# Performance work log

Measured on AMD Instinct MI355X. Metric: run time of the kernel, lower is better.

The kernel has to match this reference:

```python
import jax, jax.numpy as jnp
import numpy as np

IN_DIM = 512
OUT_DIM = 512


def setup_inputs() -> dict:
    key = jax.random.key(0)
    ks = jax.random.split(key, 7)
    B, S = 4, 2048
    scale = 1.0 / np.sqrt(IN_DIM)
    X = jax.random.normal(ks[0], (B, S, IN_DIM), dtype=jnp.float32)
    Wq = jax.random.normal(ks[1], (IN_DIM, OUT_DIM), dtype=jnp.float32) * scale
    Wk = jax.random.normal(ks[2], (IN_DIM, OUT_DIM), dtype=jnp.float32) * scale
    Wv = jax.random.normal(ks[3], (IN_DIM, OUT_DIM), dtype=jnp.float32) * scale
    bq = jnp.zeros((OUT_DIM,), dtype=jnp.float32)
    bk = jnp.zeros((OUT_DIM,), dtype=jnp.float32)
    bv = jnp.zeros((OUT_DIM,), dtype=jnp.float32)
    return {"X": X, "Wq": Wq, "bq": bq, "Wk": Wk, "bk": bk, "Wv": Wv, "bv": bv}


def reference(X, Wq, bq, Wk, bk, Wv, bv):
    # Q/K/V projections: [B,S,in] @ [in,out] -> [B,S,out]
    Q = X @ Wq + bq
    K = X @ Wk + bk
    V = X @ Wv + bv
    d_k = jnp.asarray(Q.shape[-1], Q.dtype)
    # scores: [B,S,S] = QK^T / sqrt(d_k)
    scores = jnp.einsum('bsd,btd->bst', Q, K) / jnp.sqrt(d_k)
    attn = jax.nn.softmax(scores, axis=-1)
    # out: [B,S,out]
    return jnp.einsum('bst,btd->bsd', attn, V)
```

## Files before the change

### kernel.cpp

```cpp
#include <hip/hip_runtime.h>
#include <hip/hip_bf16.h>
#include <stdint.h>

#define SEQ   2048
#define DIM   512
#define BATCH 4

typedef __attribute__((ext_vector_type(8))) short  short8;
typedef __attribute__((ext_vector_type(4))) float  floatx4;

static __device__ __forceinline__ unsigned short f2b(float f) {
  return __builtin_bit_cast(unsigned short, __float2bfloat16(f));
}

static __device__ __forceinline__ void gll16(const void* g, void* l) {
  __builtin_amdgcn_global_load_lds(
      (__attribute__((address_space(1))) void*)(uintptr_t)g,
      (__attribute__((address_space(3))) void*)l, 16, 0, 0);
}


template <int AF, int BF, int WM, int WN, int KC, int KIT>
__device__ __forceinline__ void fgemm_pipe(
    const char* __restrict__ A, int rtA0, int TKA,
    const char* __restrict__ B, int rtB0, int TKB,
    char* lds, floatx4 (&acc)[AF / WM][BF / WN])
{
  constexpr int AWF  = AF / WM, BWF = BF / WN;
  constexpr int SLOT = (AF + BF) * KC * 1024;
  constexpr int L    = KC * (AF / 8 + BF / 8);
  static_assert(KIT >= 3, "pipeline needs >=3 K-steps");
  const int tid = threadIdx.x;
  const int w = tid >> 6, l = tid & 63;
  const int wm = w % WM, wn = w / WM;

  auto stage = [&](int slot, int kt) {
    char* dst = lds + slot * SLOT;
#pragma unroll
    for (int c = 0; c < KC; ++c) {
#pragma unroll
      for (int q = 0; q < AF / 8; ++q) {
        const int f = q * 8 + w;
        gll16(A + (((size_t)(rtA0 + f) * TKA + kt * KC + c) << 10) + l * 16,
              dst + (c * AF + f) * 1024 + l * 16);
      }
#pragma unroll
      for (int q = 0; q < BF / 8; ++q) {
        const int f = q * 8 + w;
        gll16(B + (((size_t)(rtB0 + f) * TKB + kt * KC + c) << 10) + l * 16,
              dst + (KC * AF + c * BF + f) * 1024 + l * 16);
      }
    }
  };

  stage(0, 0); stage(1, 1); stage(2, 2);
  asm volatile("s_waitcnt vmcnt(%0) lgkmcnt(0)\ns_barrier" :: "n"(2 * L) : "memory");

#pragma unroll 4
  for (int kt = 0; kt < KIT; ++kt) {
    const int cslot = kt & 3;
    if (kt + 3 < KIT) stage((kt + 3) & 3, kt + 3);

    const char* bA = lds + cslot * SLOT;
    const char* bB = bA + KC * AF * 1024;
    short8 af[KC][AWF], bf[KC][BWF];
#pragma unroll
    for (int c = 0; c < KC; ++c) {
#pragma unroll
      for (int i = 0; i < AWF; ++i)
        af[c][i] = *(const short8*)(bA + (c * AF + wm * AWF + i) * 1024 + l * 16);
#pragma unroll
      for (int j = 0; j < BWF; ++j)
        bf[c][j] = *(const short8*)(bB + (c * BF + wn * BWF + j) * 1024 + l * 16);
    }
    __builtin_amdgcn_s_setprio(1);
#pragma unroll
    for (int c = 0; c < KC; ++c)
#pragma unroll
      for (int i = 0; i < AWF; ++i)
#pragma unroll
        for (int j = 0; j < BWF; ++j)
          acc[i][j] = __builtin_amdgcn_mfma_f32_16x16x32_bf16(af[c][i], bf[c][j], acc[i][j], 0, 0, 0);
    __builtin_amdgcn_s_setprio(0);

    if (kt + 1 < KIT) {
      if (kt + 3 < KIT)
        asm volatile("s_waitcnt vmcnt(%0) lgkmcnt(0)\ns_barrier" :: "n"(2 * L) : "memory");
      else if (kt + 2 < KIT)
        asm volatile("s_waitcnt vmcnt(%0) lgkmcnt(0)\ns_barrier" :: "n"(L) : "memory");
      else
        asm volatile("s_waitcnt vmcnt(0) lgkmcnt(0)\ns_barrier" ::: "memory");
    }
  }
}

__global__ __launch_bounds__(256) void setup_kernel(
    const float* __restrict__ X, const float* __restrict__ Wq,
    const float* __restrict__ Wk, const float* __restrict__ Wv,
    short8* __restrict__ XbF, short8* __restrict__ WF,
    float* __restrict__ rowsum)
{
  const int flat = blockIdx.x * 256 + threadIdx.x;
  {
    const int tile = flat >> 6, l = flat & 63;
    const int row = (tile >> 4) * 16 + (l & 15);
    const int k0  = (tile & 15) * 32 + (l >> 4) * 8;
    const float4 v0 = *(const float4*)(X + (size_t)row * DIM + k0);
    const float4 v1 = *(const float4*)(X + (size_t)row * DIM + k0 + 4);
    short8 o;
    o[0] = (short)f2b(v0.x); o[1] = (short)f2b(v0.y);
    o[2] = (short)f2b(v0.z); o[3] = (short)f2b(v0.w);
    o[4] = (short)f2b(v1.x); o[5] = (short)f2b(v1.y);
    o[6] = (short)f2b(v1.z); o[7] = (short)f2b(v1.w);
    XbF[flat] = o;
  }
  if (flat < 3 * 32768) {
    const int z = flat >> 15, within = flat & 32767;
    const float* W = (z == 0) ? Wq : (z == 1) ? Wk : Wv;
    const int tile = within >> 6, l = within & 63;
    const int n  = (tile >> 4) * 16 + (l & 15);
    const int k0 = (tile & 15) * 32 + (l >> 4) * 8;
    short8 o;
#pragma unroll
    for (int e = 0; e < 8; ++e)
      o[e] = (short)f2b(W[(size_t)(k0 + e) * DIM + n]);
    WF[flat] = o;
  }
  if (flat < 2048) ((float4*)rowsum)[flat] = float4{0.f, 0.f, 0.f, 0.f};
}

__global__ __launch_bounds__(512, 2) void qkv_kernel(
    const short8* __restrict__ XbF, const short8* __restrict__ WF,
    const float* __restrict__ bq, const float* __restrict__ bk,
    const float* __restrict__ bv,
    unsigned short* __restrict__ QF, unsigned short* __restrict__ KF,
    unsigned short* __restrict__ VF)
{
  __shared__ char lds[131072];
  const int z = blockIdx.z, job = blockIdx.x;
  const int lane = threadIdx.x & 63, w = threadIdx.x >> 6;
  const int wm = w & 1, wn = w >> 1;
  const int x = job & 31, y = job >> 5;
  const char* Xc = (const char*)XbF;
  const char* Wc = (const char*)WF;
  floatx4 acc[8][4] = {};

  if (z < 2) {
    fgemm_pipe<16, 16, 2, 4, 1, 16>(Wc + (size_t)z * 524288, y * 16, 16,
                                    Xc, x * 16, 16, lds, acc);
    const float* bias = z ? bk : bq;
    unsigned short* OF = z ? KF : QF;
    const int dbase = y * 256 + wm * 128;
    const int sbase = x * 256 + wn * 64;
#pragma unroll
    for (int i = 0; i < 8; ++i) {
      const int d0 = dbase + i * 16 + (lane >> 4) * 4;
      const float4 b4 = *(const float4*)(bias + d0);
#pragma unroll
      for (int j = 0; j < 4; ++j) {
        const int s = sbase + j * 16 + (lane & 15);
        ushort4 pk;
        pk.x = f2b(acc[i][j][0] + b4.x);
        pk.y = f2b(acc[i][j][1] + b4.y);
        pk.z = f2b(acc[i][j][2] + b4.z);
        pk.w = f2b(acc[i][j][3] + b4.w);
        *(ushort4*)(OF + (size_t)((s >> 4) * 16 + (d0 >> 5)) * 512 +
                    ((((d0 & 31) >> 3) << 4) | (s & 15)) * 8 + (d0 & 7)) = pk;
      }
    }
  } else {
    fgemm_pipe<16, 16, 2, 4, 1, 16>(Xc, x * 16, 16,
                                    Wc + 2 * 524288, y * 16, 16, lds, acc);
    const int sbase = x * 256 + wm * 128;
    const int dbase = y * 256 + wn * 64;
#pragma unroll
    for (int i = 0; i < 8; ++i) {
      const int s0 = sbase + i * 16 + (lane >> 4) * 4;
      const int bt = s0 >> 11, t0 = s0 & 2047;
#pragma unroll
      for (int j = 0; j < 4; ++j) {
        const int d = dbase + j * 16 + (lane & 15);
        const float bn = bv[d];
        ushort4 pk;
        pk.x = f2b(acc[i][j][0] + bn);
        pk.y = f2b(acc[i][j][1] + bn);
        pk.z = f2b(acc[i][j][2] + bn);
        pk.w = f2b(acc[i][j][3] + bn);
        *(ushort4*)(VF + (size_t)bt * DIM * SEQ +
                    (size_t)((d >> 4) * 64 + (t0 >> 5)) * 512 +
                    ((((t0 & 31) >> 3) << 4) | (d & 15)) * 8 + (t0 & 7)) = pk;
      }
    }
  }
}

__global__ __launch_bounds__(512, 2) void scores_kernel(
    const unsigned short* __restrict__ QF, const unsigned short* __restrict__ KF,
    unsigned short* __restrict__ ScF, float* __restrict__ rowsum)
{
  __shared__ char lds[131072];
  const int b = blockIdx.z, x = blockIdx.x, y = blockIdx.y;
  const int lane = threadIdx.x & 63, w = threadIdx.x >> 6;
  const int wm = w & 1, wn = w >> 1;
  floatx4 acc[8][4] = {};
  fgemm_pipe<16, 16, 2, 4, 1, 16>((const char*)KF + (size_t)b * 2097152, y * 16, 16,
                                  (const char*)QF + (size_t)b * 2097152, x * 16, 16,
                                  lds, acc);

  unsigned short* S = ScF + (size_t)b * SEQ * SEQ;
  const float scale = 0.044194173824159216f;
  const int tbase = y * 256 + wm * 128;
  const int sbase = x * 256 + wn * 64;
  float colsum[4] = {0.f, 0.f, 0.f, 0.f};
#pragma unroll
  for (int i = 0; i < 8; ++i) {
    const int t0 = tbase + i * 16 + (lane >> 4) * 4;
#pragma unroll
    for (int j = 0; j < 4; ++j) {
      const int s = sbase + j * 16 + (lane & 15);
      float e0 = __expf(acc[i][j][0] * scale);
      float e1 = __expf(acc[i][j][1] * scale);
      float e2 = __expf(acc[i][j][2] * scale);
      float e3 = __expf(acc[i][j][3] * scale);
      colsum[j] += (e0 + e1) + (e2 + e3);
      ushort4 pk;
      pk.x = f2b(e0); pk.y = f2b(e1); pk.z = f2b(e2); pk.w = f2b(e3);
      *(ushort4*)(S + (size_t)((s >> 4) * 64 + (t0 >> 5)) * 512 +
                  ((((t0 & 31) >> 3) << 4) | (s & 15)) * 8 + (t0 & 7)) = pk;
    }
  }
#pragma unroll
  for (int j = 0; j < 4; ++j) {
    colsum[j] += __shfl_xor(colsum[j], 16, 64);
    colsum[j] += __shfl_xor(colsum[j], 32, 64);
  }
  if (lane < 16) {
#pragma unroll
    for (int j = 0; j < 4; ++j)
      atomicAdd(rowsum + b * SEQ + sbase + j * 16 + lane, colsum[j]);
  }
}

__global__ __launch_bounds__(512, 2) void pv_kernel(
    const unsigned short* __restrict__ ScF, const unsigned short* __restrict__ VF,
    const float* __restrict__ rowsum, float* __restrict__ out)
{
  __shared__ char lds[131072];
  const int b = blockIdx.z, x = blockIdx.x, y = blockIdx.y;
  const int lane = threadIdx.x & 63, w = threadIdx.x >> 6;
  const int wm = w & 1, wn = w >> 1;
  floatx4 acc[4][2] = {};
  fgemm_pipe<8, 8, 2, 4, 2, 32>((const char*)ScF + (size_t)b * 8388608, x * 8, 64,
                                (const char*)VF + (size_t)b * 2097152, y * 8, 64,
                                lds, acc);

  const int mbase = x * 128 + wm * 64;
  const int dbase = y * 128 + wn * 32;
#pragma unroll
  for (int i = 0; i < 4; ++i) {
    const int m0 = mbase + i * 16 + (lane >> 4) * 4;
    const float4 rs = *(const float4*)(rowsum + b * SEQ + m0);
    const float inv0 = 1.f / rs.x, inv1 = 1.f / rs.y, inv2 = 1.f / rs.z, inv3 = 1.f / rs.w;
#pragma unroll
    for (int j = 0; j < 2; ++j) {
      const int d = dbase + j * 16 + (lane & 15);
      float* o = out + ((size_t)b * SEQ + m0) * DIM + d;
      o[0 * DIM] = acc[i][j][0] * inv0;
      o[1 * DIM] = acc[i][j][1] * inv1;
      o[2 * DIM] = acc[i][j][2] * inv2;
      o[3 * DIM] = acc[i][j][3] * inv3;
    }
  }
}

extern "C" void kernel_launch(void* const* d_in, const int* in_sizes, int n_in,
                              void* d_out, int out_size, void* d_ws, size_t ws_size,
                              hipStream_t stream) {
  const float* X  = (const float*)d_in[0];
  const float* Wq = (const float*)d_in[1];
  const float* bq = (const float*)d_in[2];
  const float* Wk = (const float*)d_in[3];
  const float* bk = (const float*)d_in[4];
  const float* Wv = (const float*)d_in[5];
  const float* bv = (const float*)d_in[6];
  float* out = (float*)d_out;
  char* ws = (char*)d_ws;

  short8* XbF = (short8*)(ws + 0);
  short8* WF  = (short8*)(ws + 8388608);
  char*   QF  = ws + 9961472;
  char*   KF  = ws + 18350080;
  char*   VF  = ws + 26738688;
  char*   ScF = ws + 35127296;
  float*  rowsum = (float*)(ws + 68681728);

  setup_kernel<<<dim3(2048), 256, 0, stream>>>(X, Wq, Wk, Wv, XbF, WF, rowsum);
  qkv_kernel<<<dim3(64, 1, 3), 512, 0, stream>>>(
      XbF, WF, bq, bk, bv,
      (unsigned short*)QF, (unsigned short*)KF, (unsigned short*)VF);
  scores_kernel<<<dim3(8, 8, 4), 512, 0, stream>>>(
      (const unsigned short*)QF, (const unsigned short*)KF,
      (unsigned short*)ScF, rowsum);
  pv_kernel<<<dim3(16, 4, 4), 512, 0, stream>>>(
      (const unsigned short*)ScF, (const unsigned short*)VF, rowsum, out);
}
```

Measured before the change: 146.5 us.

## Split GEMM K-step into phases interleaving LDS reads, global prefetch, and MFMA

Restructures the shared GEMM pipeline so each K-step is split into PH phases. Each phase loads part of the A fragments, issues part of the next global-to-LDS prefetch, and runs its MFMAs, with barriers between phases. B fragments are loaded once per step. The aim is to interleave memory issue with matrix work across waves and reduce register pressure from fragments held at once. The extra barriers add sync cost, and the pv kernel uses PH=1, which mostly reorders its loop.

```diff
diff --git a/kernel.cpp b/kernel.cpp
--- a/kernel.cpp
+++ b/kernel.cpp
@@ -20,8 +20,8 @@
 }
 
 
-template <int AF, int BF, int WM, int WN, int KC, int KIT>
-__device__ __forceinline__ void fgemm_pipe(
+template <int AF, int BF, int WM, int WN, int KC, int PH, int KIT>
+__device__ __forceinline__ void fgemm_8p(
     const char* __restrict__ A, int rtA0, int TKA,
     const char* __restrict__ B, int rtB0, int TKB,
     char* lds, floatx4 (&acc)[AF / WM][BF / WN])
@@ -29,67 +29,84 @@
   constexpr int AWF  = AF / WM, BWF = BF / WN;
   constexpr int SLOT = (AF + BF) * KC * 1024;
   constexpr int L    = KC * (AF / 8 + BF / 8);
-  static_assert(KIT >= 3, "pipeline needs >=3 K-steps");
+  constexpr int AC   = AWF / PH;
+  static_assert(KIT >= 3, "pipeline needs >=3 K-slots");
+  static_assert(AWF % PH == 0 && L % PH == 0, "phase split must divide");
   const int tid = threadIdx.x;
   const int w = tid >> 6, l = tid & 63;
   const int wm = w % WM, wn = w / WM;
 
-  auto stage = [&](int slot, int kt) {
+  auto stage_part = [&](int slot, int kt, int p) {
     char* dst = lds + slot * SLOT;
 #pragma unroll
-    for (int c = 0; c < KC; ++c) {
-#pragma unroll
-      for (int q = 0; q < AF / 8; ++q) {
+    for (int g = p * (L / PH); g < (p + 1) * (L / PH); ++g) {
+      if (g < KC * (AF / 8)) {
+        const int c = g / (AF / 8), q = g % (AF / 8);
         const int f = q * 8 + w;
         gll16(A + (((size_t)(rtA0 + f) * TKA + kt * KC + c) << 10) + l * 16,
               dst + (c * AF + f) * 1024 + l * 16);
-      }
-#pragma unroll
-      for (int q = 0; q < BF / 8; ++q) {
+      } else {
+        const int h = g - KC * (AF / 8);
+        const int c = h / (BF / 8), q = h % (BF / 8);
         const int f = q * 8 + w;
         gll16(B + (((size_t)(rtB0 + f) * TKB + kt * KC + c) << 10) + l * 16,
               dst + (KC * AF + c * BF + f) * 1024 + l * 16);
       }
     }
   };
-
-  stage(0, 0); stage(1, 1); stage(2, 2);
+  auto stage_all = [&](int slot, int kt) {
+#pragma unroll
+    for (int p = 0; p < PH; ++p) stage_part(slot, kt, p);
+  };
+
+  stage_all(0, 0); stage_all(1, 1); stage_all(2, 2);
   asm volatile("s_waitcnt vmcnt(%0) lgkmcnt(0)\ns_barrier" :: "n"(2 * L) : "memory");
 
+  short8 bf[KC][BWF];
 #pragma unroll 4
   for (int kt = 0; kt < KIT; ++kt) {
-    const int cslot = kt & 3;
-    if (kt + 3 < KIT) stage((kt + 3) & 3, kt + 3);
-
-    const char* bA = lds + cslot * SLOT;
+    const char* bA = lds + (kt & 3) * SLOT;
     const char* bB = bA + KC * AF * 1024;
-    short8 af[KC][AWF], bf[KC][BWF];
-#pragma unroll
-    for (int c = 0; c < KC; ++c) {
-#pragma unroll
-      for (int i = 0; i < AWF; ++i)
-        af[c][i] = *(const short8*)(bA + (c * AF + wm * AWF + i) * 1024 + l * 16);
-#pragma unroll
-      for (int j = 0; j < BWF; ++j)
-        bf[c][j] = *(const short8*)(bB + (c * BF + wn * BWF + j) * 1024 + l * 16);
-    }
-    __builtin_amdgcn_s_setprio(1);
-#pragma unroll
-    for (int c = 0; c < KC; ++c)
-#pragma unroll
-      for (int i = 0; i < AWF; ++i)
-#pragma unroll
-        for (int j = 0; j < BWF; ++j)
-          acc[i][j] = __builtin_amdgcn_mfma_f32_16x16x32_bf16(af[c][i], bf[c][j], acc[i][j], 0, 0, 0);
-    __builtin_amdgcn_s_setprio(0);
-
-    if (kt + 1 < KIT) {
-      if (kt + 3 < KIT)
-        asm volatile("s_waitcnt vmcnt(%0) lgkmcnt(0)\ns_barrier" :: "n"(2 * L) : "memory");
-      else if (kt + 2 < KIT)
-        asm volatile("s_waitcnt vmcnt(%0) lgkmcnt(0)\ns_barrier" :: "n"(L) : "memory");
-      else
-        asm volatile("s_waitcnt vmcnt(0) lgkmcnt(0)\ns_barrier" ::: "memory");
+#pragma unroll
+    for (int p = 0; p < PH; ++p) {
+      short8 af[KC][AC];
+#pragma unroll
+      for (int c = 0; c < KC; ++c)
+#pragma unroll
+        for (int i = 0; i < AC; ++i)
+          af[c][i] = *(const short8*)(bA + (c * AF + wm * AWF + p * AC + i) * 1024 + l * 16);
+      if (p == 0) {
+#pragma unroll
+        for (int c = 0; c < KC; ++c)
+#pragma unroll
+          for (int j = 0; j < BWF; ++j)
+            bf[c][j] = *(const short8*)(bB + (c * BF + wn * BWF + j) * 1024 + l * 16);
+      }
+      if (kt + 3 < KIT) stage_part((kt + 3) & 3, kt + 3, p);
+
+      asm volatile("s_barrier" ::: "memory");
+      asm volatile("s_waitcnt lgkmcnt(0)" ::: "memory");
+      __builtin_amdgcn_s_setprio(1);
+#pragma unroll
+      for (int c = 0; c < KC; ++c)
+#pragma unroll
+        for (int i = 0; i < AC; ++i)
+#pragma unroll
+          for (int j = 0; j < BWF; ++j)
+            acc[p * AC + i][j] = __builtin_amdgcn_mfma_f32_16x16x32_bf16(
+                af[c][i], bf[c][j], acc[p * AC + i][j], 0, 0, 0);
+      __builtin_amdgcn_s_setprio(0);
+
+      if (p == PH - 1) {
+        if (kt + 3 < KIT)
+          asm volatile("s_waitcnt vmcnt(%0)\ns_barrier" :: "n"(2 * L) : "memory");
+        else if (kt + 2 < KIT)
+          asm volatile("s_waitcnt vmcnt(%0)\ns_barrier" :: "n"(L) : "memory");
+        else if (kt + 1 < KIT)
+          asm volatile("s_waitcnt vmcnt(0)\ns_barrier" ::: "memory");
+      } else {
+        asm volatile("s_barrier" ::: "memory");
+      }
     }
   }
 }
@@ -146,8 +163,8 @@
   floatx4 acc[8][4] = {};
 
   if (z < 2) {
-    fgemm_pipe<16, 16, 2, 4, 1, 16>(Wc + (size_t)z * 524288, y * 16, 16,
-                                    Xc, x * 16, 16, lds, acc);
+    fgemm_8p<16, 16, 2, 4, 1, 2, 16>(Wc + (size_t)z * 524288, y * 16, 16,
+                                     Xc, x * 16, 16, lds, acc);
     const float* bias = z ? bk : bq;
     unsigned short* OF = z ? KF : QF;
     const int dbase = y * 256 + wm * 128;
@@ -169,8 +186,8 @@
       }
     }
   } else {
-    fgemm_pipe<16, 16, 2, 4, 1, 16>(Xc, x * 16, 16,
-                                    Wc + 2 * 524288, y * 16, 16, lds, acc);
+    fgemm_8p<16, 16, 2, 4, 1, 2, 16>(Xc, x * 16, 16,
+                                     Wc + 2 * 524288, y * 16, 16, lds, acc);
     const int sbase = x * 256 + wm * 128;
     const int dbase = y * 256 + wn * 64;
 #pragma unroll
@@ -203,9 +220,9 @@
   const int lane = threadIdx.x & 63, w = threadIdx.x >> 6;
   const int wm = w & 1, wn = w >> 1;
   floatx4 acc[8][4] = {};
-  fgemm_pipe<16, 16, 2, 4, 1, 16>((const char*)KF + (size_t)b * 2097152, y * 16, 16,
-                                  (const char*)QF + (size_t)b * 2097152, x * 16, 16,
-                                  lds, acc);
+  fgemm_8p<16, 16, 2, 4, 1, 2, 16>((const char*)KF + (size_t)b * 2097152, y * 16, 16,
+                                   (const char*)QF + (size_t)b * 2097152, x * 16, 16,
+                                   lds, acc);
 
   unsigned short* S = ScF + (size_t)b * SEQ * SEQ;
   const float scale = 0.044194173824159216f;
@@ -250,9 +267,9 @@
   const int lane = threadIdx.x & 63, w = threadIdx.x >> 6;
   const int wm = w & 1, wn = w >> 1;
   floatx4 acc[4][2] = {};
-  fgemm_pipe<8, 8, 2, 4, 2, 32>((const char*)ScF + (size_t)b * 8388608, x * 8, 64,
-                                (const char*)VF + (size_t)b * 2097152, y * 8, 64,
-                                lds, acc);
+  fgemm_8p<8, 8, 2, 4, 2, 1, 32>((const char*)ScF + (size_t)b * 8388608, x * 8, 64,
+                                 (const char*)VF + (size_t)b * 2097152, y * 8, 64,
+                                 lds, acc);
 
   const int mbase = x * 128 + wm * 64;
   const int dbase = y * 128 + wn * 32;
```

Measured after the change: 140.7 us. -4.0%, faster.
